# Kernel optimization log

Measured on AMD Instinct MI355X. Metric: run time of the kernel, lower is better.

The kernel has to match this reference:

```python
import jax, jax.numpy as jnp
from jax import lax
import numpy as np
import math

IN_SHAPE = [2, 4, 4]   # factorize(32, 4)
OUT_SHAPE = [2, 4, 4]
RANK = 8
GROUPS = 1
KH = KW = 3
OUT_CH = 32
IN_CH = 32


def setup_inputs() -> dict:
    key = jax.random.key(0)
    ks = jax.random.split(key, 6)

    def uni(k, shape, bound):
        return jax.random.uniform(k, shape, jnp.float32, -bound, bound)

    kernels = []
    for l in range(3):
        fi, fo = IN_SHAPE[l], OUT_SHAPE[l]
        bound = math.sqrt(6.0 / (fi + fo))
        kernels.append(uni(ks[l], (IN_SHAPE[l], OUT_SHAPE[l], RANK), bound))
    bound = math.sqrt(6.0 / (KH * KW * RANK + KH * KW))
    k3 = uni(ks[3], (GROUPS, KH, KW, RANK), bound)

    x = jax.random.normal(ks[4], (8, IN_CH, 512, 512), dtype=jnp.float32)
    bias = jnp.zeros((OUT_CH,), dtype=jnp.float32)
    return {"x": x, "k0": kernels[0], "k1": kernels[1], "k2": kernels[2],
            "k3": k3, "bias": bias}


def reference(x, k0, k1, k2, k3, bias):
    # CP weight reconstruction (chained einsums, as in the torch module)
    wl = jnp.einsum('iar,jbr->ijabr', k0, k1)          # [2,2,4,4,R]
    wr = jnp.einsum('kcr,ghwr->ghwkcr', k2, k3)        # [1,3,3,4,4,R]
    w = jnp.einsum('ijabr,ghwkcr->gijkabchw', wl, wr)  # [1,2,4,4,2,4,4,3,3]
    w = w.reshape(OUT_CH, IN_CH // GROUPS, KH, KW)     # [O, I, 3, 3]
    # flip + true convolution in conv_einsum == cross-correlation with w;
    # 'max'-mode output then [1:-1] trim == valid conv of the pad-1 input.
    out = lax.conv_general_dilated(
        x, w, window_strides=(1, 1), padding=((1, 1), (1, 1)),
        dimension_numbers=('NCHW', 'OIHW', 'NCHW'),
        feature_group_count=GROUPS)
    out = out + bias[None, :, None, None]
    return out  # [batch, out_channels, 512, 512]
```

## Files before the change

kernel.cpp:

```cpp
#include <hip/hip_runtime.h>
#include <hip/hip_bf16.h>

#define H 512
#define W 512
#define C 32
#define O 32
#define TW 64
#define TH 4

using bf16x8 = __attribute__((ext_vector_type(8))) short;
using f32x4  = __attribute__((ext_vector_type(4))) float;

__device__ __forceinline__ unsigned short f2bf(float f) {
    union { float f; unsigned u; } c; c.f = f;
    unsigned r = c.u + 0x7fffu + ((c.u >> 16) & 1u);
    return (unsigned short)(r >> 16);
}

__global__ void recon_w(const float* __restrict__ k0, const float* __restrict__ k1,
                        const float* __restrict__ k2, const float* __restrict__ k3,
                        unsigned short* __restrict__ wout) {
    int idx = blockIdx.x * 256 + threadIdx.x;
    if (idx >= 9 * 32 * 32) return;
    int ci = idx & 31;
    int o  = (idx >> 5) & 31;
    int s  = idx >> 10;
    int i = o >> 4, j = (o >> 2) & 3, k = o & 3;
    int a = ci >> 4, b = (ci >> 2) & 3, c = ci & 3;
    float acc = 0.f;
    #pragma unroll
    for (int r = 0; r < 8; ++r)
        acc += k0[(i*2 + a)*8 + r] * k1[(j*4 + b)*8 + r]
             * k2[(k*4 + c)*8 + r] * k3[s*8 + r];
    wout[idx] = f2bf(acc);
}

__launch_bounds__(256, 4)
__global__ void conv_mfma(const float* __restrict__ x,
                          const unsigned short* __restrict__ wq,
                          const float* __restrict__ bias,
                          float* __restrict__ out) {
    __shared__ __align__(16) unsigned short sx[TH + 2][TW + 2][C];

    const int tid = threadIdx.x;
    const int bid = blockIdx.x;
    const int n  = bid >> 10;
    const int r2 = bid & 1023;
    const int ty = r2 >> 3;
    const int tx = r2 & 7;
    const int y0 = ty * TH, x0 = tx * TW;

    const int lane = tid & 63;
    const int pix  = lane & 15;
    const int quad = lane >> 4;

    bf16x8 bw[9][2];
    #pragma unroll
    for (int s = 0; s < 9; ++s)
        #pragma unroll
        for (int h = 0; h < 2; ++h)
            bw[s][h] = *(const bf16x8*)(wq + ((s*32 + h*16 + pix)*32 + quad*8));

    for (int task = tid; task < (TH + 2) * 4 * (TW + 2); task += 256) {
        int gxl = task % (TW + 2);
        int t2  = task / (TW + 2);
        int ciq = t2 & 3;
        int row = t2 >> 2;
        int gy = y0 + row - 1;
        int gx = x0 + gxl - 1;
        bool inb = (gy >= 0) && (gy < H) && (gx >= 0) && (gx < W);
        const float* p = x + (((n*C + ciq*8)*H + gy)*W + gx);
        float v[8];
        #pragma unroll
        for (int j2 = 0; j2 < 8; ++j2) v[j2] = inb ? p[j2 * H * W] : 0.f;
        uint4 pk;
        pk.x = (unsigned)f2bf(v[0]) | ((unsigned)f2bf(v[1]) << 16);
        pk.y = (unsigned)f2bf(v[2]) | ((unsigned)f2bf(v[3]) << 16);
        pk.z = (unsigned)f2bf(v[4]) | ((unsigned)f2bf(v[5]) << 16);
        pk.w = (unsigned)f2bf(v[6]) | ((unsigned)f2bf(v[7]) << 16);
        int pos = ciq ^ ((gxl >> 1) & 3);
        *(uint4*)&sx[row][gxl][pos * 8] = pk;
    }
    __syncthreads();

    const int wave = tid >> 6;
    const float b0 = bias[pix];
    const float b1 = bias[16 + pix];
    const int wrow = wave;

    #pragma unroll
    for (int mt = 0; mt < 4; ++mt) {
        const int xm = mt << 4;
        f32x4 acc0 = {0.f, 0.f, 0.f, 0.f};
        f32x4 acc1 = {0.f, 0.f, 0.f, 0.f};
        #pragma unroll
        for (int s = 0; s < 9; ++s) {
            const int dy = s / 3, dx = s % 3;
            const int xp = xm + pix + dx;
            const int pos = quad ^ ((xp >> 1) & 3);
            bf16x8 a = *(const bf16x8*)&sx[wrow + dy][xp][pos * 8];
            acc0 = __builtin_amdgcn_mfma_f32_16x16x32_bf16(a, bw[s][0], acc0, 0, 0, 0);
            acc1 = __builtin_amdgcn_mfma_f32_16x16x32_bf16(a, bw[s][1], acc1, 0, 0, 0);
        }
        const int gy = y0 + wrow;
        const int base0 = ((n*O + pix)      * H + gy) * W + x0 + xm + quad * 4;
        const int base1 = ((n*O + 16 + pix) * H + gy) * W + x0 + xm + quad * 4;
        f32x4 v0 = acc0 + b0;
        f32x4 v1 = acc1 + b1;
        *(f32x4*)(out + base0) = v0;
        *(f32x4*)(out + base1) = v1;
    }
}

extern "C" void kernel_launch(void* const* d_in, const int* in_sizes, int n_in,
                              void* d_out, int out_size, void* d_ws, size_t ws_size,
                              hipStream_t stream) {
    const float* x    = (const float*)d_in[0];
    const float* k0   = (const float*)d_in[1];
    const float* k1   = (const float*)d_in[2];
    const float* k2   = (const float*)d_in[3];
    const float* k3   = (const float*)d_in[4];
    const float* bias = (const float*)d_in[5];
    float* out = (float*)d_out;
    unsigned short* wbuf = (unsigned short*)d_ws;

    recon_w<<<36, 256, 0, stream>>>(k0, k1, k2, k3, wbuf);
    conv_mfma<<<8192, 256, 0, stream>>>(x, wbuf, bias, out);
}
```

Measured before the change: 511.2 us.

## Stream taller row strips through an LDS ring buffer with register prefetch

Each block now covers 16 output rows instead of 4. It keeps a 12-row LDS ring and loads the next 4 input rows plus halo columns into registers while the MFMA work for the current 4 rows runs. This cuts the vertical halo reloads (from 6/4 toward 18/16) and overlaps global loads with compute. In exchange there are 4x fewer blocks, more registers per thread (occupancy hint lowered to 3), larger LDS use, and extra barriers per strip.

Measured after the change: 478.6 us. 1.07x faster.

```diff
diff --git a/kernel.cpp b/kernel.cpp
--- a/kernel.cpp
+++ b/kernel.cpp
@@ -7,6 +7,9 @@
 #define O 32
 #define TW 64
 #define TH 4
+#define SH 16
+#define NS 4
+#define RING 12
 
 using bf16x8 = __attribute__((ext_vector_type(8))) short;
 using f32x4  = __attribute__((ext_vector_type(4))) float;
@@ -15,6 +18,15 @@
     union { float f; unsigned u; } c; c.f = f;
     unsigned r = c.u + 0x7fffu + ((c.u >> 16) & 1u);
     return (unsigned short)(r >> 16);
+}
+
+__device__ __forceinline__ uint4 pack8(const float* v) {
+    uint4 pk;
+    pk.x = (unsigned)f2bf(v[0]) | ((unsigned)f2bf(v[1]) << 16);
+    pk.y = (unsigned)f2bf(v[2]) | ((unsigned)f2bf(v[3]) << 16);
+    pk.z = (unsigned)f2bf(v[4]) | ((unsigned)f2bf(v[5]) << 16);
+    pk.w = (unsigned)f2bf(v[6]) | ((unsigned)f2bf(v[7]) << 16);
+    return pk;
 }
 
 __global__ void recon_w(const float* __restrict__ k0, const float* __restrict__ k1,
@@ -35,22 +47,22 @@
     wout[idx] = f2bf(acc);
 }
 
-__launch_bounds__(256, 4)
+__launch_bounds__(256, 3)
 __global__ void conv_mfma(const float* __restrict__ x,
                           const unsigned short* __restrict__ wq,
                           const float* __restrict__ bias,
                           float* __restrict__ out) {
-    __shared__ __align__(16) unsigned short sx[TH + 2][TW + 2][C];
+    __shared__ __align__(16) unsigned short sx[RING][TW + 2][C];
 
     const int tid = threadIdx.x;
     const int bid = blockIdx.x;
-    const int n  = bid >> 10;
-    const int r2 = bid & 1023;
-    const int ty = r2 >> 3;
-    const int tx = r2 & 7;
-    const int y0 = ty * TH, x0 = tx * TW;
+    const int n  = bid >> 8;
+    const int ty = (bid >> 3) & 31;
+    const int tx = bid & 7;
+    const int y0 = ty * SH, x0 = tx * TW;
 
     const int lane = tid & 63;
+    const int wave = tid >> 6;
     const int pix  = lane & 15;
     const int quad = lane >> 4;
 
@@ -61,54 +73,96 @@
         for (int h = 0; h < 2; ++h)
             bw[s][h] = *(const bf16x8*)(wq + ((s*32 + h*16 + pix)*32 + quad*8));
 
-    for (int task = tid; task < (TH + 2) * 4 * (TW + 2); task += 256) {
-        int gxl = task % (TW + 2);
-        int t2  = task / (TW + 2);
+    for (int task = tid; task < 6 * 4 * 66; task += 256) {
+        int gxl = task % 66;
+        int t2  = task / 66;
         int ciq = t2 & 3;
-        int row = t2 >> 2;
-        int gy = y0 + row - 1;
+        int r   = t2 >> 2;
+        int gy = y0 - 1 + r;
         int gx = x0 + gxl - 1;
-        bool inb = (gy >= 0) && (gy < H) && (gx >= 0) && (gx < W);
+        bool inb = (gy >= 0) && (gx >= 0) && (gx < W);
         const float* p = x + (((n*C + ciq*8)*H + gy)*W + gx);
         float v[8];
         #pragma unroll
         for (int j2 = 0; j2 < 8; ++j2) v[j2] = inb ? p[j2 * H * W] : 0.f;
-        uint4 pk;
-        pk.x = (unsigned)f2bf(v[0]) | ((unsigned)f2bf(v[1]) << 16);
-        pk.y = (unsigned)f2bf(v[2]) | ((unsigned)f2bf(v[3]) << 16);
-        pk.z = (unsigned)f2bf(v[4]) | ((unsigned)f2bf(v[5]) << 16);
-        pk.w = (unsigned)f2bf(v[6]) | ((unsigned)f2bf(v[7]) << 16);
         int pos = ciq ^ ((gxl >> 1) & 3);
-        *(uint4*)&sx[row][gxl][pos * 8] = pk;
+        *(uint4*)&sx[r][gxl][pos * 8] = pack8(v);
     }
     __syncthreads();
 
-    const int wave = tid >> 6;
     const float b0 = bias[pix];
     const float b1 = bias[16 + pix];
-    const int wrow = wave;
 
     #pragma unroll
-    for (int mt = 0; mt < 4; ++mt) {
-        const int xm = mt << 4;
-        f32x4 acc0 = {0.f, 0.f, 0.f, 0.f};
-        f32x4 acc1 = {0.f, 0.f, 0.f, 0.f};
+    for (int s = 0; s < NS; ++s) {
+        const int rbase = (4 * s) % RING;
+
+        float v[4][8];
+        float vh[8];
+        int hcol = 0, hciq = 0, hrow = 0;
+        if (s + 1 < NS) {
+            #pragma unroll
+            for (int k = 0; k < 4; ++k) {
+                int gy = y0 + 4*s + 5 + k;
+                bool inb = (gy < H);
+                const float* p = x + (((n*C + wave*8)*H + gy)*W + x0 + lane);
+                #pragma unroll
+                for (int j2 = 0; j2 < 8; ++j2)
+                    v[k][j2] = inb ? p[j2 * H * W] : 0.f;
+            }
+            if (tid < 32) {
+                hcol = (tid & 1) ? 65 : 0;
+                hciq = (tid >> 1) & 3;
+                hrow = tid >> 3;
+                int gy = y0 + 4*s + 5 + hrow;
+                int gx = x0 + hcol - 1;
+                bool inb = (gy < H) && (gx >= 0) && (gx < W);
+                const float* p = x + (((n*C + hciq*8)*H + gy)*W + gx);
+                #pragma unroll
+                for (int j2 = 0; j2 < 8; ++j2)
+                    vh[j2] = inb ? p[j2 * H * W] : 0.f;
+            }
+        }
+
+        const int gy_out = y0 + 4*s + wave;
         #pragma unroll
-        for (int s = 0; s < 9; ++s) {
-            const int dy = s / 3, dx = s % 3;
-            const int xp = xm + pix + dx;
-            const int pos = quad ^ ((xp >> 1) & 3);
-            bf16x8 a = *(const bf16x8*)&sx[wrow + dy][xp][pos * 8];
-            acc0 = __builtin_amdgcn_mfma_f32_16x16x32_bf16(a, bw[s][0], acc0, 0, 0, 0);
-            acc1 = __builtin_amdgcn_mfma_f32_16x16x32_bf16(a, bw[s][1], acc1, 0, 0, 0);
+        for (int mt = 0; mt < 4; ++mt) {
+            const int xm = mt << 4;
+            f32x4 acc0 = {0.f, 0.f, 0.f, 0.f};
+            f32x4 acc1 = {0.f, 0.f, 0.f, 0.f};
+            #pragma unroll
+            for (int stp = 0; stp < 9; ++stp) {
+                const int dy = stp / 3, dx = stp % 3;
+                int sl = rbase + wave + dy; if (sl >= RING) sl -= RING;
+                const int xp = xm + pix + dx;
+                const int pos = quad ^ ((xp >> 1) & 3);
+                bf16x8 a = *(const bf16x8*)&sx[sl][xp][pos * 8];
+                acc0 = __builtin_amdgcn_mfma_f32_16x16x32_bf16(a, bw[stp][0], acc0, 0, 0, 0);
+                acc1 = __builtin_amdgcn_mfma_f32_16x16x32_bf16(a, bw[stp][1], acc1, 0, 0, 0);
+            }
+            const int base0 = ((n*O + pix     ) * H + gy_out) * W + x0 + xm + quad*4;
+            const int base1 = ((n*O + 16 + pix) * H + gy_out) * W + x0 + xm + quad*4;
+            f32x4 o0 = acc0 + b0;
+            f32x4 o1 = acc1 + b1;
+            *(f32x4*)(out + base0) = o0;
+            *(f32x4*)(out + base1) = o1;
         }
-        const int gy = y0 + wrow;
-        const int base0 = ((n*O + pix)      * H + gy) * W + x0 + xm + quad * 4;
-        const int base1 = ((n*O + 16 + pix) * H + gy) * W + x0 + xm + quad * 4;
-        f32x4 v0 = acc0 + b0;
-        f32x4 v1 = acc1 + b1;
-        *(f32x4*)(out + base0) = v0;
-        *(f32x4*)(out + base1) = v1;
+
+        if (s + 1 < NS) {
+            #pragma unroll
+            for (int k = 0; k < 4; ++k) {
+                int sl = rbase + 6 + k; if (sl >= RING) sl -= RING;
+                int gxl = lane + 1;
+                int pos = wave ^ ((gxl >> 1) & 3);
+                *(uint4*)&sx[sl][gxl][pos * 8] = pack8(v[k]);
+            }
+            if (tid < 32) {
+                int sl = rbase + 6 + hrow; if (sl >= RING) sl -= RING;
+                int pos = hciq ^ ((hcol >> 1) & 3);
+                *(uint4*)&sx[sl][hcol][pos * 8] = pack8(vh);
+            }
+            __syncthreads();
+        }
     }
 }
 
@@ -125,5 +179,5 @@
     unsigned short* wbuf = (unsigned short*)d_ws;
 
     recon_w<<<36, 256, 0, stream>>>(k0, k1, k2, k3, wbuf);
-    conv_mfma<<<8192, 256, 0, stream>>>(x, wbuf, bias, out);
+    conv_mfma<<<2048, 256, 0, stream>>>(x, wbuf, bias, out);
 }
```

## Stream row strips through an LDS ring buffer with register-prefetched loads

Applied to the files above, without the earlier changes.

Each block now covers a 32x32 tile and walks down it in 4-row steps. Input rows sit in a 10-row LDS ring, so the halo rows are reused between steps instead of being reloaded per 4-row tile. Global loads for the next step go into registers while MFMA runs on the current step, and the block index is swizzled across batch images. Each wave now does one output-channel half over two rows, with s_setprio raised around the MFMA chain. This adds complexity in ring indexing, halo handling and register pressure.

Result: slower. 580.6 us (+13.6%).

```diff
diff --git a/kernel.cpp b/kernel.cpp
--- a/kernel.cpp
+++ b/kernel.cpp
@@ -5,8 +5,11 @@
 #define W 512
 #define C 32
 #define O 32
-#define TW 64
-#define TH 4
+#define TW 32
+#define SH 32
+#define NS 8
+#define RING 10
+#define XCOLS (TW + 2)
 
 using bf16x8 = __attribute__((ext_vector_type(8))) short;
 using f32x4  = __attribute__((ext_vector_type(4))) float;
@@ -15,6 +18,22 @@
     union { float f; unsigned u; } c; c.f = f;
     unsigned r = c.u + 0x7fffu + ((c.u >> 16) & 1u);
     return (unsigned short)(r >> 16);
+}
+
+__device__ __forceinline__ uint4 pack8(const float* v) {
+    uint4 pk;
+    pk.x = (unsigned)f2bf(v[0]) | ((unsigned)f2bf(v[1]) << 16);
+    pk.y = (unsigned)f2bf(v[2]) | ((unsigned)f2bf(v[3]) << 16);
+    pk.z = (unsigned)f2bf(v[4]) | ((unsigned)f2bf(v[5]) << 16);
+    pk.w = (unsigned)f2bf(v[6]) | ((unsigned)f2bf(v[7]) << 16);
+    return pk;
+}
+
+__device__ __forceinline__ uint2 pack4(const float* v) {
+    uint2 pk;
+    pk.x = (unsigned)f2bf(v[0]) | ((unsigned)f2bf(v[1]) << 16);
+    pk.y = (unsigned)f2bf(v[2]) | ((unsigned)f2bf(v[3]) << 16);
+    return pk;
 }
 
 __global__ void recon_w(const float* __restrict__ k0, const float* __restrict__ k1,
@@ -35,80 +54,150 @@
     wout[idx] = f2bf(acc);
 }
 
+
+#define ISSUE(VM, VH, SW) do {                                              \
+    _Pragma("unroll")                                                       \
+    for (int rp = 0; rp < 2; ++rp) {                                        \
+        int gy = y0 + 4*(SW) + 5 + 2*rp + half;                             \
+        bool inb = (gy < H);                                                \
+        const float* p = x + (((n*C + wave*8)*H + gy)*W + x0 + col);        \
+        _Pragma("unroll")                                                   \
+        for (int j2 = 0; j2 < 8; ++j2) VM[rp][j2] = inb ? p[j2*H*W] : 0.f;  \
+    }                                                                       \
+    if (tid < 64) {                                                         \
+        int gy = y0 + 4*(SW) + 5 + hrow;                                    \
+        bool inb = (gy < H) && hx_ok;                                       \
+        const float* p = x + (((n*C + hciq*8 + hh*4)*H + gy)*W + hgx);      \
+        _Pragma("unroll")                                                   \
+        for (int j2 = 0; j2 < 4; ++j2) VH[j2] = inb ? p[j2*H*W] : 0.f;      \
+    }                                                                       \
+} while (0)
+
+#define WRITE(VM, VH, RB) do {                                              \
+    _Pragma("unroll")                                                       \
+    for (int rp = 0; rp < 2; ++rp) {                                        \
+        int k = 2*rp + half;                                                \
+        int sl = (RB) + 6 + k; if (sl >= RING) sl -= RING;                  \
+        int gxl = col + 1;                                                  \
+        int pos = wave ^ ((gxl >> 1) & 3);                                  \
+        *(uint4*)&sx[sl][gxl][pos * 8] = pack8(VM[rp]);                     \
+    }                                                                       \
+    if (tid < 64) {                                                         \
+        int sl = (RB) + 6 + hrow; if (sl >= RING) sl -= RING;               \
+        int pos = hciq ^ ((hcol >> 1) & 3);                                 \
+        *(uint2*)&sx[sl][hcol][pos * 8 + hh * 4] = pack4(VH);               \
+    }                                                                       \
+    __syncthreads();                                                        \
+} while (0)
+
+#define COMPUTE(S, RB) do {                                                 \
+    _Pragma("unroll")                                                       \
+    for (int rr = 0; rr < 2; ++rr) {                                        \
+        const int row = 2*wr + rr;                                          \
+        f32x4 accA = {0.f,0.f,0.f,0.f};                                     \
+        f32x4 accB = {0.f,0.f,0.f,0.f};                                     \
+        __builtin_amdgcn_s_setprio(1);                                      \
+        _Pragma("unroll")                                                   \
+        for (int dy = 0; dy < 3; ++dy) {                                    \
+            int sl = (RB) + row + dy; if (sl >= RING) sl -= RING;           \
+            _Pragma("unroll")                                               \
+            for (int dx = 0; dx < 3; ++dx) {                                \
+                const int stp = dy * 3 + dx;                                \
+                const int xpA = pix + dx;                                   \
+                const int xpB = 16 + pix + dx;                              \
+                const int posA = quad ^ ((xpA >> 1) & 3);                   \
+                const int posB = quad ^ ((xpB >> 1) & 3);                   \
+                bf16x8 a0 = *(const bf16x8*)&sx[sl][xpA][posA * 8];         \
+                bf16x8 a1 = *(const bf16x8*)&sx[sl][xpB][posB * 8];         \
+                accA = __builtin_amdgcn_mfma_f32_16x16x32_bf16(a0, bw[stp], accA, 0, 0, 0); \
+                accB = __builtin_amdgcn_mfma_f32_16x16x32_bf16(a1, bw[stp], accB, 0, 0, 0); \
+            }                                                               \
+        }                                                                   \
+        __builtin_amdgcn_s_setprio(0);                                      \
+        const int gy_out = y0 + 4*(S) + row;                                \
+        const int base = ((n*O + oh*16 + pix) * H + gy_out) * W + x0 + quad*4; \
+        f32x4 oA = accA + bz;                                               \
+        f32x4 oB = accB + bz;                                               \
+        *(f32x4*)(out + base)      = oA;                                    \
+        *(f32x4*)(out + base + 16) = oB;                                    \
+    }                                                                       \
+} while (0)
+
 __launch_bounds__(256, 4)
 __global__ void conv_mfma(const float* __restrict__ x,
                           const unsigned short* __restrict__ wq,
                           const float* __restrict__ bias,
                           float* __restrict__ out) {
-    __shared__ __align__(16) unsigned short sx[TH + 2][TW + 2][C];
+    __shared__ __align__(16) unsigned short sx[RING][XCOLS][C];
 
     const int tid = threadIdx.x;
-    const int bid = blockIdx.x;
-    const int n  = bid >> 10;
-    const int r2 = bid & 1023;
-    const int ty = r2 >> 3;
-    const int tx = r2 & 7;
-    const int y0 = ty * TH, x0 = tx * TW;
+    const int bid = ((blockIdx.x & 7) << 8) | (blockIdx.x >> 3);
+    const int n  = bid >> 8;
+    const int ty = (bid >> 4) & 15;
+    const int tx = bid & 15;
+    const int y0 = ty * SH, x0 = tx * TW;
 
     const int lane = tid & 63;
+    const int wave = tid >> 6;
     const int pix  = lane & 15;
     const int quad = lane >> 4;
-
-    bf16x8 bw[9][2];
+    const int col  = lane & 31;
+    const int half = lane >> 5;
+    const int wr = wave >> 1;
+    const int oh = wave & 1;
+
+    const int hcol = (tid & 1) ? (XCOLS - 1) : 0;
+    const int hh   = (tid >> 1) & 1;
+    const int hciq = (tid >> 2) & 3;
+    const int hrow = tid >> 4;
+    const int hgx0 = x0 + hcol - 1;
+    const bool hx_ok = (hgx0 >= 0) && (hgx0 < W);
+    const int hgx = hx_ok ? hgx0 : 0;
+
+    bf16x8 bw[9];
     #pragma unroll
     for (int s = 0; s < 9; ++s)
-        #pragma unroll
-        for (int h = 0; h < 2; ++h)
-            bw[s][h] = *(const bf16x8*)(wq + ((s*32 + h*16 + pix)*32 + quad*8));
-
-    for (int task = tid; task < (TH + 2) * 4 * (TW + 2); task += 256) {
-        int gxl = task % (TW + 2);
-        int t2  = task / (TW + 2);
+        bw[s] = *(const bf16x8*)(wq + ((s*32 + oh*16 + pix)*32 + quad*8));
+
+    for (int task = tid; task < 6 * 4 * XCOLS; task += 256) {
+        int gxl = task % XCOLS;
+        int t2  = task / XCOLS;
         int ciq = t2 & 3;
-        int row = t2 >> 2;
-        int gy = y0 + row - 1;
+        int r   = t2 >> 2;
+        int gy = y0 - 1 + r;
         int gx = x0 + gxl - 1;
-        bool inb = (gy >= 0) && (gy < H) && (gx >= 0) && (gx < W);
+        bool inb = (gy >= 0) && (gx >= 0) && (gx < W);
         const float* p = x + (((n*C + ciq*8)*H + gy)*W + gx);
         float v[8];
         #pragma unroll
         for (int j2 = 0; j2 < 8; ++j2) v[j2] = inb ? p[j2 * H * W] : 0.f;
-        uint4 pk;
-        pk.x = (unsigned)f2bf(v[0]) | ((unsigned)f2bf(v[1]) << 16);
-        pk.y = (unsigned)f2bf(v[2]) | ((unsigned)f2bf(v[3]) << 16);
-        pk.z = (unsigned)f2bf(v[4]) | ((unsigned)f2bf(v[5]) << 16);
-        pk.w = (unsigned)f2bf(v[6]) | ((unsigned)f2bf(v[7]) << 16);
         int pos = ciq ^ ((gxl >> 1) & 3);
-        *(uint4*)&sx[row][gxl][pos * 8] = pk;
+        *(uint4*)&sx[r][gxl][pos * 8] = pack8(v);
     }
+
+    const float bz = bias[oh * 16 + pix];
+
+    float vmA[2][8], vhA[4];
+    float vmB[2][8], vhB[4];
+
+    ISSUE(vmA, vhA, 0);
+    __builtin_amdgcn_sched_barrier(0);
     __syncthreads();
 
-    const int wave = tid >> 6;
-    const float b0 = bias[pix];
-    const float b1 = bias[16 + pix];
-    const int wrow = wave;
-
     #pragma unroll
-    for (int mt = 0; mt < 4; ++mt) {
-        const int xm = mt << 4;
-        f32x4 acc0 = {0.f, 0.f, 0.f, 0.f};
-        f32x4 acc1 = {0.f, 0.f, 0.f, 0.f};
-        #pragma unroll
-        for (int s = 0; s < 9; ++s) {
-            const int dy = s / 3, dx = s % 3;
-            const int xp = xm + pix + dx;
-            const int pos = quad ^ ((xp >> 1) & 3);
-            bf16x8 a = *(const bf16x8*)&sx[wrow + dy][xp][pos * 8];
-            acc0 = __builtin_amdgcn_mfma_f32_16x16x32_bf16(a, bw[s][0], acc0, 0, 0, 0);
-            acc1 = __builtin_amdgcn_mfma_f32_16x16x32_bf16(a, bw[s][1], acc1, 0, 0, 0);
-        }
-        const int gy = y0 + wrow;
-        const int base0 = ((n*O + pix)      * H + gy) * W + x0 + xm + quad * 4;
-        const int base1 = ((n*O + 16 + pix) * H + gy) * W + x0 + xm + quad * 4;
-        f32x4 v0 = acc0 + b0;
-        f32x4 v1 = acc1 + b1;
-        *(f32x4*)(out + base0) = v0;
-        *(f32x4*)(out + base1) = v1;
+    for (int su = 0; su < NS; su += 2) {
+        const int rb0 = (4 * su) % RING;
+        const int rb1 = (4 * su + 4) % RING;
+
+        if (su + 2 < NS) ISSUE(vmB, vhB, su + 1);
+        __builtin_amdgcn_sched_barrier(0);
+        COMPUTE(su, rb0);
+        WRITE(vmA, vhA, rb0);
+
+        if (su + 3 < NS) ISSUE(vmA, vhA, su + 2);
+        __builtin_amdgcn_sched_barrier(0);
+        COMPUTE(su + 1, rb1);
+        if (su + 2 < NS) WRITE(vmB, vhB, rb1);
     }
 }
 
@@ -125,5 +214,5 @@
     unsigned short* wbuf = (unsigned short*)d_ws;
 
     recon_w<<<36, 256, 0, stream>>>(k0, k1, k2, k3, wbuf);
-    conv_mfma<<<8192, 256, 0, stream>>>(x, wbuf, bias, out);
-}
+    conv_mfma<<<2048, 256, 0, stream>>>(x, wbuf, bias, out);
+}
```
